# Performance work log

Measured on AMD Instinct MI355X. Metric: run time of the kernel, lower is better.

Reference implementation:

```python
import jax, jax.numpy as jnp
import numpy as np

N_NODES = 50000
N_EDGES = 800000
HIDDEN = 128          # hidden_dim
MSG = HIDDEN // 2     # message_dim = LSTM hidden size


def setup_inputs() -> dict:
    key = jax.random.key(0)
    ks = jax.random.split(key, 9)
    feat = jax.random.normal(ks[0], (N_NODES, HIDDEN), dtype=jnp.float32)
    src0 = jax.random.randint(ks[1], (N_EDGES,), 0, N_NODES, dtype=jnp.int32)
    dst0 = jax.random.randint(ks[2], (N_EDGES,), 0, N_NODES, dtype=jnp.int32)
    src1 = jax.random.randint(ks[3], (N_EDGES,), 0, N_NODES, dtype=jnp.int32)
    dst1 = jax.random.randint(ks[4], (N_EDGES,), 0, N_NODES, dtype=jnp.int32)
    # PyTorch LSTMCell params: gates order (i, f, g, o), scale 1/sqrt(hidden)
    s = 1.0 / np.sqrt(MSG)
    W_ih = jax.random.uniform(ks[5], (4 * MSG, HIDDEN), jnp.float32, -s, s)
    W_hh = jax.random.uniform(ks[6], (4 * MSG, MSG), jnp.float32, -s, s)
    b_ih = jax.random.uniform(ks[7], (4 * MSG,), jnp.float32, -s, s)
    b_hh = jax.random.uniform(ks[8], (4 * MSG,), jnp.float32, -s, s)
    return {"feat": feat, "src0": src0, "dst0": dst0, "src1": src1,
            "dst1": dst1, "W_ih": W_ih, "W_hh": W_hh, "b_ih": b_ih, "b_hh": b_hh}


def _etype_mean(feat, src, dst, n_nodes):
    """copy_u('h','m') + mean('m','ft') for one edge type."""
    m = feat[src]                                             # [E, H] gather
    s = jax.ops.segment_sum(m, dst, num_segments=n_nodes)    # [N, H]
    cnt = jax.ops.segment_sum(jnp.ones(src.shape, feat.dtype), dst,
                              num_segments=n_nodes)          # [N]
    mean = s / jnp.maximum(cnt, 1.0)[:, None]
    return mean, (cnt > 0).astype(feat.dtype)


def reference(feat, src0, dst0, src1, dst1, W_ih, W_hh, b_ih, b_hh):
    n = feat.shape[0]
    ft0, has0 = _etype_mean(feat, src0, dst0, n)
    ft1, has1 = _etype_mean(feat, src1, dst1, n)
    # cross_reducer='mean': average over etypes that delivered messages
    n_active = jnp.maximum(has0 + has1, 1.0)[:, None]
    rst = (ft0 + ft1) / n_active                              # [N, H]

    G_t = rst[:, :MSG]   # h0
    R_t = rst[:, MSG:]   # c0

    # PyTorch LSTMCell: gates = x W_ih^T + b_ih + h W_hh^T + b_hh
    gates = feat @ W_ih.T + b_ih + G_t @ W_hh.T + b_hh       # [N, 4*MSG]
    i, f, g, o = jnp.split(gates, 4, axis=1)
    c1 = jax.nn.sigmoid(f) * R_t + jax.nn.sigmoid(i) * jnp.tanh(g)
    h1 = jax.nn.sigmoid(o) * jnp.tanh(c1)
    return jnp.concatenate([h1, c1], axis=1)                  # [N, H]
```

## Files before the change

kernel.cpp:

```cpp
#include <hip/hip_runtime.h>
#include <hip/hip_fp16.h>
#include <cmath>

#define NN 50000
#define NE 800000
#define NPB 32
#define NBKT 196
#define BKT_SHIFT 8
#define BKT_NODES 256
#define BKT_CAP 6144
#define CHUNK 4096
#define NCH 196

using f16x8 = __attribute__((ext_vector_type(8))) _Float16;
using f32x4 = __attribute__((ext_vector_type(4))) float;

__device__ __forceinline__ float sigmoidf_(float x) {
    return 1.0f / (1.0f + __expf(-x));
}
__device__ __forceinline__ float tanhf_(float x) {
    float t = __expf(-2.0f * fabsf(x));
    float r = (1.0f - t) / (1.0f + t);
    return copysignf(r, x);
}

__global__ __launch_bounds__(256) void prep_kernel(
    const float* __restrict__ feat, __half* __restrict__ feat_h,
    const float* __restrict__ Wih, const float* __restrict__ Whh,
    const float* __restrict__ b_ih, const float* __restrict__ b_hh,
    __half* __restrict__ WC, float* __restrict__ bsum,
    int* __restrict__ bcnt) {
    int i = blockIdx.x * blockDim.x + threadIdx.x;

    {
        const float4 v = ((const float4*)feat)[i];
        __half2 lo = __floats2half2_rn(v.x, v.y);
        __half2 hi = __floats2half2_rn(v.z, v.w);
        ((__half2*)feat_h)[2 * i]     = lo;
        ((__half2*)feat_h)[2 * i + 1] = hi;
    }
    if (i < 256 * 128) {
        int g = i >> 7, k = i & 127;
        WC[(size_t)g * 192 + k] = __float2half(Wih[i]);
    }
    if (i < 256 * 64) {
        int g = i >> 6, k = i & 63;
        WC[(size_t)g * 192 + 128 + k] = __float2half(Whh[i]);
    }
    if (i < 256) bsum[i] = b_ih[i] + b_hh[i];
    if (i < 2 * NBKT) bcnt[i] = 0;
}

__global__ __launch_bounds__(256) void bin_kernel(
    const int* __restrict__ src0, const int* __restrict__ dst0,
    const int* __restrict__ src1, const int* __restrict__ dst1,
    int* __restrict__ bcnt,
    unsigned* __restrict__ binned0, unsigned* __restrict__ binned1) {
    __shared__ int cnt[NBKT];
    __shared__ int base[NBKT];
    __shared__ int cur[NBKT];
    __shared__ int sdst[CHUNK];

    int x  = blockIdx.x;
    int et = x >= NCH;
    int c  = et ? x - NCH : x;
    const int* src = et ? src1 : src0;
    const int* dst = et ? dst1 : dst0;
    unsigned* binned = et ? binned1 : binned0;

    int start = c * CHUNK;
    int n = min(CHUNK, NE - start);
    int tid = threadIdx.x;

    if (tid < NBKT) { cnt[tid] = 0; cur[tid] = 0; }
    __syncthreads();
    for (int i = tid; i < n; i += 256) {
        int d = dst[start + i];
        sdst[i] = d;
        atomicAdd(&cnt[d >> BKT_SHIFT], 1);
    }
    __syncthreads();
    if (tid < NBKT && cnt[tid] > 0)
        base[tid] = atomicAdd(&bcnt[et * NBKT + tid], cnt[tid]);
    __syncthreads();
    for (int i = tid; i < n; i += 256) {
        int d = sdst[i];
        int b = d >> BKT_SHIFT;
        int r = atomicAdd(&cur[b], 1);
        binned[(size_t)b * BKT_CAP + base[b] + r] =
            ((unsigned)d << 16) | (unsigned)src[start + i];
    }
}

__global__ __launch_bounds__(256) void bucket_scatter_kernel(
    const unsigned* __restrict__ binned0, const unsigned* __restrict__ binned1,
    const int* __restrict__ bcnt,
    int* __restrict__ off0, int* __restrict__ off1,
    int* __restrict__ deg0, int* __restrict__ deg1,
    unsigned short* __restrict__ es0, unsigned short* __restrict__ es1) {
    __shared__ int lcnt[BKT_NODES];
    __shared__ int lbase[BKT_NODES];

    int g  = blockIdx.x;
    int et = g >= NBKT;
    int b  = et ? g - NBKT : g;
    const unsigned* binned = (et ? binned1 : binned0) + (size_t)b * BKT_CAP;
    int* off = et ? off1 : off0;
    int* deg = et ? deg1 : deg0;
    unsigned short* es = (et ? es1 : es0) + (size_t)b * BKT_CAP;

    int bn = bcnt[g];
    int node0 = b * BKT_NODES;
    int tid = threadIdx.x;

    lcnt[tid] = 0;
    __syncthreads();
    for (int i = tid; i < bn; i += 256) {
        unsigned u = binned[i];
        int d = (int)(u >> 16) - node0;
        atomicAdd(&lcnt[d], 1);
    }
    __syncthreads();
    int cntv = lcnt[tid];
    for (int d = 1; d < BKT_NODES; d <<= 1) {
        int v = (tid >= d) ? lcnt[tid - d] : 0;
        __syncthreads();
        lcnt[tid] += v;
        __syncthreads();
    }
    int excl = lcnt[tid] - cntv;
    lbase[tid] = excl;
    int gn = node0 + tid;
    if (gn < NN) { off[gn] = b * BKT_CAP + excl; deg[gn] = cntv; }
    __syncthreads();
    for (int i = tid; i < bn; i += 256) {
        unsigned u = binned[i];
        int d = (int)(u >> 16) - node0;
        int r = atomicAdd(&lbase[d], 1);
        es[r] = (unsigned short)(u & 0xffffu);
    }
}

__global__ __launch_bounds__(256) void gather_kernel(
    const uint2* __restrict__ featu,
    const unsigned short* __restrict__ es0, const int* __restrict__ off0, const int* __restrict__ deg0,
    const unsigned short* __restrict__ es1, const int* __restrict__ off1, const int* __restrict__ deg1,
    uint2* __restrict__ rstu) {
    int wid  = (blockIdx.x * blockDim.x + threadIdx.x) >> 6;
    int lane = threadIdx.x & 63;
    if (wid >= NN) return;
    int hf = lane >> 5;
    int c  = lane & 31;

    float a0[4] = {0.f, 0.f, 0.f, 0.f};
    float a1[4] = {0.f, 0.f, 0.f, 0.f};

    int d0 = deg0[wid], o0 = off0[wid];
    int e = 0;
    for (; e + 8 <= d0; e += 8) {
        int s0 = es0[o0 + e + 0 + hf];
        int s1 = es0[o0 + e + 2 + hf];
        int s2 = es0[o0 + e + 4 + hf];
        int s3 = es0[o0 + e + 6 + hf];
        uint2 v0 = featu[(size_t)s0 * 32 + c];
        uint2 v1 = featu[(size_t)s1 * 32 + c];
        uint2 v2 = featu[(size_t)s2 * 32 + c];
        uint2 v3 = featu[(size_t)s3 * 32 + c];
#pragma unroll
        for (int k = 0; k < 1; k++) { }
        {
            float2 f;
            f = __half22float2(*(__half2*)&v0.x); a0[0] += f.x; a0[1] += f.y;
            f = __half22float2(*(__half2*)&v0.y); a0[2] += f.x; a0[3] += f.y;
            f = __half22float2(*(__half2*)&v1.x); a0[0] += f.x; a0[1] += f.y;
            f = __half22float2(*(__half2*)&v1.y); a0[2] += f.x; a0[3] += f.y;
            f = __half22float2(*(__half2*)&v2.x); a0[0] += f.x; a0[1] += f.y;
            f = __half22float2(*(__half2*)&v2.y); a0[2] += f.x; a0[3] += f.y;
            f = __half22float2(*(__half2*)&v3.x); a0[0] += f.x; a0[1] += f.y;
            f = __half22float2(*(__half2*)&v3.y); a0[2] += f.x; a0[3] += f.y;
        }
    }
    if (e < d0) {
        int last = d0 - 1;
#pragma unroll
        for (int j = 0; j < 4; j++) {
            int ee = e + 2 * j + hf;
            int s = es0[o0 + min(ee, last)];
            uint2 v = featu[(size_t)s * 32 + c];
            float m = (ee < d0) ? 1.f : 0.f;
            float2 f;
            f = __half22float2(*(__half2*)&v.x); a0[0] = fmaf(f.x, m, a0[0]); a0[1] = fmaf(f.y, m, a0[1]);
            f = __half22float2(*(__half2*)&v.y); a0[2] = fmaf(f.x, m, a0[2]); a0[3] = fmaf(f.y, m, a0[3]);
        }
    }

    int d1 = deg1[wid], o1 = off1[wid];
    e = 0;
    for (; e + 8 <= d1; e += 8) {
        int s0 = es1[o1 + e + 0 + hf];
        int s1 = es1[o1 + e + 2 + hf];
        int s2 = es1[o1 + e + 4 + hf];
        int s3 = es1[o1 + e + 6 + hf];
        uint2 v0 = featu[(size_t)s0 * 32 + c];
        uint2 v1 = featu[(size_t)s1 * 32 + c];
        uint2 v2 = featu[(size_t)s2 * 32 + c];
        uint2 v3 = featu[(size_t)s3 * 32 + c];
        {
            float2 f;
            f = __half22float2(*(__half2*)&v0.x); a1[0] += f.x; a1[1] += f.y;
            f = __half22float2(*(__half2*)&v0.y); a1[2] += f.x; a1[3] += f.y;
            f = __half22float2(*(__half2*)&v1.x); a1[0] += f.x; a1[1] += f.y;
            f = __half22float2(*(__half2*)&v1.y); a1[2] += f.x; a1[3] += f.y;
            f = __half22float2(*(__half2*)&v2.x); a1[0] += f.x; a1[1] += f.y;
            f = __half22float2(*(__half2*)&v2.y); a1[2] += f.x; a1[3] += f.y;
            f = __half22float2(*(__half2*)&v3.x); a1[0] += f.x; a1[1] += f.y;
            f = __half22float2(*(__half2*)&v3.y); a1[2] += f.x; a1[3] += f.y;
        }
    }
    if (e < d1) {
        int last = d1 - 1;
#pragma unroll
        for (int j = 0; j < 4; j++) {
            int ee = e + 2 * j + hf;
            int s = es1[o1 + min(ee, last)];
            uint2 v = featu[(size_t)s * 32 + c];
            float m = (ee < d1) ? 1.f : 0.f;
            float2 f;
            f = __half22float2(*(__half2*)&v.x); a1[0] = fmaf(f.x, m, a1[0]); a1[1] = fmaf(f.y, m, a1[1]);
            f = __half22float2(*(__half2*)&v.y); a1[2] = fmaf(f.x, m, a1[2]); a1[3] = fmaf(f.y, m, a1[3]);
        }
    }

#pragma unroll
    for (int k = 0; k < 4; k++) {
        a0[k] += __shfl_xor(a0[k], 32, 64);
        a1[k] += __shfl_xor(a1[k], 32, 64);
    }

    if (hf == 0) {
        float inv0 = 1.0f / fmaxf((float)d0, 1.0f);
        float inv1 = 1.0f / fmaxf((float)d1, 1.0f);
        float na = fmaxf((float)((d0 > 0) + (d1 > 0)), 1.0f);
        float r0 = (a0[0] * inv0 + a1[0] * inv1) / na;
        float r1 = (a0[1] * inv0 + a1[1] * inv1) / na;
        float r2 = (a0[2] * inv0 + a1[2] * inv1) / na;
        float r3 = (a0[3] * inv0 + a1[3] * inv1) / na;
        __half2 h01 = __floats2half2_rn(r0, r1);
        __half2 h23 = __floats2half2_rn(r2, r3);
        uint2 o;
        o.x = *(unsigned*)&h01;
        o.y = *(unsigned*)&h23;
        rstu[(size_t)wid * 32 + c] = o;
    }
}

__global__ __launch_bounds__(256) void node_kernel(
    const __half* __restrict__ feat_h,
    const __half* __restrict__ rst_h,
    const __half* __restrict__ WC, const float* __restrict__ bsum,
    float* __restrict__ out) {
    __shared__ __half xs[32 * 200];

    int t  = threadIdx.x;
    int nb = blockIdx.x * NPB;
    int lane = t & 63;
    int w    = t >> 6;
    int col  = lane & 15;
    int g4   = lane >> 4;

    f16x8 bfr[4][6];
    float bias[4];
#pragma unroll
    for (int ct = 0; ct < 4; ct++) {
        int gate = ct * 64 + w * 16 + col;
        bias[ct] = bsum[gate];
#pragma unroll
        for (int ks = 0; ks < 6; ks++)
            bfr[ct][ks] = *(const f16x8*)(WC + (size_t)gate * 192 + ks * 32 + g4 * 8);
    }

    const uint4* feat4 = (const uint4*)feat_h;
    const uint4* rst4  = (const uint4*)rst_h;
#pragma unroll
    for (int j = 0; j < 2; j++) {
        int e = t + j * 256;
        int n = e >> 4, q = e & 15;
        int gn = nb + n;
        uint4 v = make_uint4(0, 0, 0, 0);
        if (gn < NN) v = feat4[(size_t)gn * 16 + q];
        *(uint4*)(&xs[n * 200 + q * 8]) = v;
    }
    {
        int n = t >> 3, q = t & 7;
        int gn = nb + n;
        uint4 v = make_uint4(0, 0, 0, 0);
        if (gn < NN) v = rst4[(size_t)gn * 16 + q];
        *(uint4*)(&xs[n * 200 + 128 + q * 8]) = v;
    }
    __syncthreads();

    f32x4 acc[2][4];
#pragma unroll
    for (int rt = 0; rt < 2; rt++)
#pragma unroll
        for (int ct = 0; ct < 4; ct++)
            acc[rt][ct] = (f32x4){bias[ct], bias[ct], bias[ct], bias[ct]};

#pragma unroll
    for (int ks = 0; ks < 6; ks++) {
        f16x8 a0 = *(const f16x8*)(&xs[(col) * 200 + ks * 32 + g4 * 8]);
        f16x8 a1 = *(const f16x8*)(&xs[(16 + col) * 200 + ks * 32 + g4 * 8]);
#pragma unroll
        for (int ct = 0; ct < 4; ct++) {
            acc[0][ct] = __builtin_amdgcn_mfma_f32_16x16x32_f16(a0, bfr[ct][ks], acc[0][ct], 0, 0, 0);
            acc[1][ct] = __builtin_amdgcn_mfma_f32_16x16x32_f16(a1, bfr[ct][ks], acc[1][ct], 0, 0, 0);
        }
    }

    int m = w * 16 + col;
#pragma unroll
    for (int rt = 0; rt < 2; rt++) {
#pragma unroll
        for (int r = 0; r < 4; r++) {
            int nl = rt * 16 + g4 * 4 + r;
            int gn = nb + nl;
            if (gn >= NN) continue;
            float iv = sigmoidf_(acc[rt][0][r]);
            float fv = sigmoidf_(acc[rt][1][r]);
            float gv = tanhf_(acc[rt][2][r]);
            float ov = sigmoidf_(acc[rt][3][r]);
            float R  = __half2float(rst_h[(size_t)gn * 128 + 64 + m]);
            float c1 = fv * R + iv * gv;
            float h1 = ov * tanhf_(c1);
            out[(size_t)gn * 128 + m]      = h1;
            out[(size_t)gn * 128 + 64 + m] = c1;
        }
    }
}

extern "C" void kernel_launch(void* const* d_in, const int* in_sizes, int n_in,
                              void* d_out, int out_size, void* d_ws, size_t ws_size,
                              hipStream_t stream) {
    const float* feat = (const float*)d_in[0];
    const int*   src0 = (const int*)d_in[1];
    const int*   dst0 = (const int*)d_in[2];
    const int*   src1 = (const int*)d_in[3];
    const int*   dst1 = (const int*)d_in[4];
    const float* W_ih = (const float*)d_in[5];
    const float* W_hh = (const float*)d_in[6];
    const float* b_ih = (const float*)d_in[7];
    const float* b_hh = (const float*)d_in[8];
    float* out = (float*)d_out;

    char* p = (char*)d_ws;
    int* bcnt = (int*)p;            p += 2 * NBKT * 4;
    int* off0 = (int*)p;            p += NN * 4;
    int* off1 = (int*)p;            p += NN * 4;
    int* deg0 = (int*)p;            p += NN * 4;
    int* deg1 = (int*)p;            p += NN * 4;
    unsigned* binned0 = (unsigned*)p; p += (size_t)NBKT * BKT_CAP * 4;
    unsigned* binned1 = (unsigned*)p; p += (size_t)NBKT * BKT_CAP * 4;
    unsigned short* es0 = (unsigned short*)p; p += (size_t)NBKT * BKT_CAP * 2;
    unsigned short* es1 = (unsigned short*)p; p += (size_t)NBKT * BKT_CAP * 2;
    __half* feat_h = (__half*)p;    p += (size_t)NN * 128 * 2;
    __half* rst_h  = (__half*)p;    p += (size_t)NN * 128 * 2;
    __half* WC     = (__half*)p;    p += (size_t)256 * 192 * 2;
    float*  bsum   = (float*)p;     p += 256 * 4;

    int blocksP = (NN * 128 / 4 + 255) / 256;
    prep_kernel<<<blocksP, 256, 0, stream>>>(feat, feat_h, W_ih, W_hh, b_ih, b_hh,
                                             WC, bsum, bcnt);

    bin_kernel<<<2 * NCH, 256, 0, stream>>>(src0, dst0, src1, dst1, bcnt,
                                            binned0, binned1);

    bucket_scatter_kernel<<<2 * NBKT, 256, 0, stream>>>(binned0, binned1, bcnt,
                                                        off0, off1, deg0, deg1,
                                                        es0, es1);

    int blocksG = (NN * 64 + 255) / 256;
    gather_kernel<<<blocksG, 256, 0, stream>>>((const uint2*)feat_h,
                                               es0, off0, deg0, es1, off1, deg1,
                                               (uint2*)rst_h);

    int blocksN = (NN + NPB - 1) / NPB;
    node_kernel<<<blocksN, 256, 0, stream>>>(feat_h, rst_h, WC, bsum, out);
}
```

Baseline: 139.1 us.

## Split feature gather into four column-block passes over a transposed fp16 feature copy

Prep now also writes a column-blocked copy of the fp16 features, four blocks of 32 columns each stored contiguously, so every pass gathers from a 3.2 MB table that can stay in cache. The gather becomes four kernel launches, one per column block, with eight lanes per edge and eight edges in flight per wave, followed by extra shuffle reductions. Edge-index loads and the result store use nontemporal hints. The cost is reading the edge lists four times, three extra launches, and writing an extra 12.8 MB copy in prep.

```diff
diff --git a/kernel.cpp b/kernel.cpp
--- a/kernel.cpp
+++ b/kernel.cpp
@@ -24,8 +24,20 @@
     return copysignf(r, x);
 }
 
+__device__ __forceinline__ void accR(uint2 v, float* a) {
+    float2 f;
+    f = __half22float2(*(__half2*)&v.x); a[0] += f.x; a[1] += f.y;
+    f = __half22float2(*(__half2*)&v.y); a[2] += f.x; a[3] += f.y;
+}
+__device__ __forceinline__ void accRm(uint2 v, float m, float* a) {
+    float2 f;
+    f = __half22float2(*(__half2*)&v.x); a[0] = fmaf(f.x, m, a[0]); a[1] = fmaf(f.y, m, a[1]);
+    f = __half22float2(*(__half2*)&v.y); a[2] = fmaf(f.x, m, a[2]); a[3] = fmaf(f.y, m, a[3]);
+}
+
 __global__ __launch_bounds__(256) void prep_kernel(
     const float* __restrict__ feat, __half* __restrict__ feat_h,
+    uint2* __restrict__ fqt,
     const float* __restrict__ Wih, const float* __restrict__ Whh,
     const float* __restrict__ b_ih, const float* __restrict__ b_hh,
     __half* __restrict__ WC, float* __restrict__ bsum,
@@ -38,6 +50,14 @@
         __half2 hi = __floats2half2_rn(v.z, v.w);
         ((__half2*)feat_h)[2 * i]     = lo;
         ((__half2*)feat_h)[2 * i + 1] = hi;
+        int n  = i >> 5;
+        int f4 = i & 31;
+        int cb = f4 >> 3;
+        int w  = f4 & 7;
+        uint2 u;
+        u.x = *(unsigned*)&lo;
+        u.y = *(unsigned*)&hi;
+        fqt[(size_t)cb * NN * 8 + (size_t)n * 8 + w] = u;
     }
     if (i < 256 * 128) {
         int g = i >> 7, k = i & 127;
@@ -141,116 +161,85 @@
     }
 }
 
-__global__ __launch_bounds__(256) void gather_kernel(
-    const uint2* __restrict__ featu,
+__global__ __launch_bounds__(256) void gather_pass_kernel(
+    const uint2* __restrict__ fqt,
     const unsigned short* __restrict__ es0, const int* __restrict__ off0, const int* __restrict__ deg0,
     const unsigned short* __restrict__ es1, const int* __restrict__ off1, const int* __restrict__ deg1,
-    uint2* __restrict__ rstu) {
+    unsigned long long* __restrict__ rstu, int cb) {
     int wid  = (blockIdx.x * blockDim.x + threadIdx.x) >> 6;
     int lane = threadIdx.x & 63;
     if (wid >= NN) return;
-    int hf = lane >> 5;
-    int c  = lane & 31;
+    int sub = lane >> 3;
+    int c   = lane & 7;
 
     float a0[4] = {0.f, 0.f, 0.f, 0.f};
     float a1[4] = {0.f, 0.f, 0.f, 0.f};
 
     int d0 = deg0[wid], o0 = off0[wid];
     int e = 0;
-    for (; e + 8 <= d0; e += 8) {
-        int s0 = es0[o0 + e + 0 + hf];
-        int s1 = es0[o0 + e + 2 + hf];
-        int s2 = es0[o0 + e + 4 + hf];
-        int s3 = es0[o0 + e + 6 + hf];
-        uint2 v0 = featu[(size_t)s0 * 32 + c];
-        uint2 v1 = featu[(size_t)s1 * 32 + c];
-        uint2 v2 = featu[(size_t)s2 * 32 + c];
-        uint2 v3 = featu[(size_t)s3 * 32 + c];
-#pragma unroll
-        for (int k = 0; k < 1; k++) { }
-        {
-            float2 f;
-            f = __half22float2(*(__half2*)&v0.x); a0[0] += f.x; a0[1] += f.y;
-            f = __half22float2(*(__half2*)&v0.y); a0[2] += f.x; a0[3] += f.y;
-            f = __half22float2(*(__half2*)&v1.x); a0[0] += f.x; a0[1] += f.y;
-            f = __half22float2(*(__half2*)&v1.y); a0[2] += f.x; a0[3] += f.y;
-            f = __half22float2(*(__half2*)&v2.x); a0[0] += f.x; a0[1] += f.y;
-            f = __half22float2(*(__half2*)&v2.y); a0[2] += f.x; a0[3] += f.y;
-            f = __half22float2(*(__half2*)&v3.x); a0[0] += f.x; a0[1] += f.y;
-            f = __half22float2(*(__half2*)&v3.y); a0[2] += f.x; a0[3] += f.y;
-        }
+    for (; e + 16 <= d0; e += 16) {
+        int sa = __builtin_nontemporal_load(&es0[o0 + e + sub]);
+        int sb = __builtin_nontemporal_load(&es0[o0 + e + 8 + sub]);
+        uint2 va = fqt[(size_t)sa * 8 + c];
+        uint2 vb = fqt[(size_t)sb * 8 + c];
+        accR(va, a0);
+        accR(vb, a0);
     }
     if (e < d0) {
         int last = d0 - 1;
 #pragma unroll
-        for (int j = 0; j < 4; j++) {
-            int ee = e + 2 * j + hf;
-            int s = es0[o0 + min(ee, last)];
-            uint2 v = featu[(size_t)s * 32 + c];
-            float m = (ee < d0) ? 1.f : 0.f;
-            float2 f;
-            f = __half22float2(*(__half2*)&v.x); a0[0] = fmaf(f.x, m, a0[0]); a0[1] = fmaf(f.y, m, a0[1]);
-            f = __half22float2(*(__half2*)&v.y); a0[2] = fmaf(f.x, m, a0[2]); a0[3] = fmaf(f.y, m, a0[3]);
+        for (int j = 0; j < 2; j++) {
+            int ee = e + 8 * j + sub;
+            int s = __builtin_nontemporal_load(&es0[o0 + min(ee, last)]);
+            uint2 v = fqt[(size_t)s * 8 + c];
+            accRm(v, (ee < d0) ? 1.f : 0.f, a0);
         }
     }
 
     int d1 = deg1[wid], o1 = off1[wid];
     e = 0;
-    for (; e + 8 <= d1; e += 8) {
-        int s0 = es1[o1 + e + 0 + hf];
-        int s1 = es1[o1 + e + 2 + hf];
-        int s2 = es1[o1 + e + 4 + hf];
-        int s3 = es1[o1 + e + 6 + hf];
-        uint2 v0 = featu[(size_t)s0 * 32 + c];
-        uint2 v1 = featu[(size_t)s1 * 32 + c];
-        uint2 v2 = featu[(size_t)s2 * 32 + c];
-        uint2 v3 = featu[(size_t)s3 * 32 + c];
-        {
-            float2 f;
-            f = __half22float2(*(__half2*)&v0.x); a1[0] += f.x; a1[1] += f.y;
-            f = __half22float2(*(__half2*)&v0.y); a1[2] += f.x; a1[3] += f.y;
-            f = __half22float2(*(__half2*)&v1.x); a1[0] += f.x; a1[1] += f.y;
-            f = __half22float2(*(__half2*)&v1.y); a1[2] += f.x; a1[3] += f.y;
-            f = __half22float2(*(__half2*)&v2.x); a1[0] += f.x; a1[1] += f.y;
-            f = __half22float2(*(__half2*)&v2.y); a1[2] += f.x; a1[3] += f.y;
-            f = __half22float2(*(__half2*)&v3.x); a1[0] += f.x; a1[1] += f.y;
-            f = __half22float2(*(__half2*)&v3.y); a1[2] += f.x; a1[3] += f.y;
-        }
+    for (; e + 16 <= d1; e += 16) {
+        int sa = __builtin_nontemporal_load(&es1[o1 + e + sub]);
+        int sb = __builtin_nontemporal_load(&es1[o1 + e + 8 + sub]);
+        uint2 va = fqt[(size_t)sa * 8 + c];
+        uint2 vb = fqt[(size_t)sb * 8 + c];
+        accR(va, a1);
+        accR(vb, a1);
     }
     if (e < d1) {
         int last = d1 - 1;
 #pragma unroll
-        for (int j = 0; j < 4; j++) {
-            int ee = e + 2 * j + hf;
-            int s = es1[o1 + min(ee, last)];
-            uint2 v = featu[(size_t)s * 32 + c];
-            float m = (ee < d1) ? 1.f : 0.f;
-            float2 f;
-            f = __half22float2(*(__half2*)&v.x); a1[0] = fmaf(f.x, m, a1[0]); a1[1] = fmaf(f.y, m, a1[1]);
-            f = __half22float2(*(__half2*)&v.y); a1[2] = fmaf(f.x, m, a1[2]); a1[3] = fmaf(f.y, m, a1[3]);
+        for (int j = 0; j < 2; j++) {
+            int ee = e + 8 * j + sub;
+            int s = __builtin_nontemporal_load(&es1[o1 + min(ee, last)]);
+            uint2 v = fqt[(size_t)s * 8 + c];
+            accRm(v, (ee < d1) ? 1.f : 0.f, a1);
         }
     }
 
 #pragma unroll
     for (int k = 0; k < 4; k++) {
+        a0[k] += __shfl_xor(a0[k], 8, 64);
+        a0[k] += __shfl_xor(a0[k], 16, 64);
         a0[k] += __shfl_xor(a0[k], 32, 64);
+        a1[k] += __shfl_xor(a1[k], 8, 64);
+        a1[k] += __shfl_xor(a1[k], 16, 64);
         a1[k] += __shfl_xor(a1[k], 32, 64);
     }
 
-    if (hf == 0) {
+    if (lane < 8) {
         float inv0 = 1.0f / fmaxf((float)d0, 1.0f);
         float inv1 = 1.0f / fmaxf((float)d1, 1.0f);
         float na = fmaxf((float)((d0 > 0) + (d1 > 0)), 1.0f);
-        float r0 = (a0[0] * inv0 + a1[0] * inv1) / na;
-        float r1 = (a0[1] * inv0 + a1[1] * inv1) / na;
-        float r2 = (a0[2] * inv0 + a1[2] * inv1) / na;
-        float r3 = (a0[3] * inv0 + a1[3] * inv1) / na;
-        __half2 h01 = __floats2half2_rn(r0, r1);
-        __half2 h23 = __floats2half2_rn(r2, r3);
-        uint2 o;
-        o.x = *(unsigned*)&h01;
-        o.y = *(unsigned*)&h23;
-        rstu[(size_t)wid * 32 + c] = o;
+        float v0 = (a0[0] * inv0 + a1[0] * inv1) / na;
+        float v1 = (a0[1] * inv0 + a1[1] * inv1) / na;
+        float v2 = (a0[2] * inv0 + a1[2] * inv1) / na;
+        float v3 = (a0[3] * inv0 + a1[3] * inv1) / na;
+        __half2 h01 = __floats2half2_rn(v0, v1);
+        __half2 h23 = __floats2half2_rn(v2, v3);
+        unsigned long long o = ((unsigned long long)(*(unsigned*)&h23) << 32)
+                             | (unsigned long long)(*(unsigned*)&h01);
+        __builtin_nontemporal_store(o, &rstu[(size_t)wid * 32 + cb * 8 + lane]);
     }
 }
 
@@ -363,12 +352,14 @@
     unsigned short* es0 = (unsigned short*)p; p += (size_t)NBKT * BKT_CAP * 2;
     unsigned short* es1 = (unsigned short*)p; p += (size_t)NBKT * BKT_CAP * 2;
     __half* feat_h = (__half*)p;    p += (size_t)NN * 128 * 2;
+    uint2*  fqt    = (uint2*)p;     p += (size_t)NN * 32 * 8;
     __half* rst_h  = (__half*)p;    p += (size_t)NN * 128 * 2;
     __half* WC     = (__half*)p;    p += (size_t)256 * 192 * 2;
     float*  bsum   = (float*)p;     p += 256 * 4;
 
     int blocksP = (NN * 128 / 4 + 255) / 256;
-    prep_kernel<<<blocksP, 256, 0, stream>>>(feat, feat_h, W_ih, W_hh, b_ih, b_hh,
+    prep_kernel<<<blocksP, 256, 0, stream>>>(feat, feat_h, fqt,
+                                             W_ih, W_hh, b_ih, b_hh,
                                              WC, bsum, bcnt);
 
     bin_kernel<<<2 * NCH, 256, 0, stream>>>(src0, dst0, src1, dst1, bcnt,
@@ -379,9 +370,12 @@
                                                         es0, es1);
 
     int blocksG = (NN * 64 + 255) / 256;
-    gather_kernel<<<blocksG, 256, 0, stream>>>((const uint2*)feat_h,
-                                               es0, off0, deg0, es1, off1, deg1,
-                                               (uint2*)rst_h);
+    for (int cb = 0; cb < 4; cb++) {
+        gather_pass_kernel<<<blocksG, 256, 0, stream>>>(
+            fqt + (size_t)cb * NN * 8,
+            es0, off0, deg0, es1, off1, deg1,
+            (unsigned long long*)rst_h, cb);
+    }
 
     int blocksN = (NN + NPB - 1) / NPB;
     node_kernel<<<blocksN, 256, 0, stream>>>(feat_h, rst_h, WC, bsum, out);
```

Measured after the change: 212.0 us. +52.4%, slower.
